# Kernel tuning notes

Measured on AMD Instinct MI355X. Metric: run time of the kernel, lower is better.

## Reference

```python
import jax, jax.numpy as jnp
import numpy as np

N_HEAD = 16
SCALE = float(np.sqrt(1024 // N_HEAD))  # source multiplies by sqrt(head_dim) (faithful to bug)


def setup_inputs() -> dict:
    key = jax.random.key(0)
    ks = jax.random.split(key, 4)
    B, T, D = 4, 2048, 1024
    std = 1.0 / np.sqrt(D)
    return {
        "x": jax.random.normal(ks[0], (B, T, D), dtype=jnp.float32),
        "Wq": jax.random.normal(ks[1], (D, D), dtype=jnp.float32) * std,
        "bq": jnp.zeros((D,), dtype=jnp.float32),
        "Wk": jax.random.normal(ks[2], (D, D), dtype=jnp.float32) * std,
        "bk": jnp.zeros((D,), dtype=jnp.float32),
        "Wv": jax.random.normal(ks[3], (D, D), dtype=jnp.float32) * std,
        "bv": jnp.zeros((D,), dtype=jnp.float32),
    }


def reference(x, Wq, bq, Wk, bk, Wv, bv):
    B, T, D = x.shape
    H = N_HEAD
    hd = D // H
    # linear projections (torch Linear: x @ W^T + b)
    q = x @ Wq.T + bq
    k = x @ Wk.T + bk
    v = x @ Wv.T + bv
    # [B, H, T, hd]
    q = q.reshape(B, T, H, hd).transpose(0, 2, 1, 3)
    k = k.reshape(B, T, H, hd).transpose(0, 2, 1, 3)
    v = v.reshape(B, T, H, hd).transpose(0, 2, 1, 3)
    # scores [B, H, T, T]; note: source MULTIPLIES by sqrt(head_dim)
    att = jnp.einsum("bhqd,bhkd->bhqk", q, k) * SCALE
    causal = jnp.tril(jnp.ones((T, T), dtype=bool))
    att = jnp.where(causal, att, -jnp.inf)
    att = jax.nn.softmax(att, axis=-1)
    y = jnp.einsum("bhqk,bhkd->bhqd", att, v)
    return y.transpose(0, 2, 1, 3).reshape(B, T, D)
```

## Files before the change

### kernel.cpp

```cpp
#include <hip/hip_runtime.h>
#include <math.h>

#define TSEQ   2048
#define NBATCH 4
#define NHEAD  16
#define HDIM   64
#define DMODEL 1024
#define MROWS  (NBATCH * TSEQ)
#define QSCALE 11.541560327111707f

typedef float f32x4  __attribute__((ext_vector_type(4)));
typedef short bf16x8 __attribute__((ext_vector_type(8)));
typedef _Float16 f16x8 __attribute__((ext_vector_type(8)));

static __device__ __forceinline__ short f2bf(float f) {
    union { float f; unsigned u; } a; a.f = f;
    unsigned r = a.u + 0x7FFFu + ((a.u >> 16) & 1u);
    return (short)(r >> 16);
}
static __device__ __forceinline__ float bf2f(short s) {
    union { unsigned u; float f; } a; a.u = ((unsigned)(unsigned short)s) << 16;
    return a.f;
}

static __device__ __forceinline__ void async_copy16(void* lds, const void* g) {
    __builtin_amdgcn_global_load_lds(
        (const __attribute__((address_space(1))) void*)g,
        (__attribute__((address_space(3))) void*)lds, 16, 0, 0);
}

#define X_F4 (MROWS * DMODEL / 4)
#define W_F4 (DMODEL * DMODEL / 4)
__global__ __launch_bounds__(256) void split_all(
    const float* __restrict__ x,
    const float* __restrict__ wq, const float* __restrict__ wk,
    const float* __restrict__ wv,
    short* __restrict__ Xhi, short* __restrict__ Xlo,
    short* __restrict__ Whi, short* __restrict__ Wlo)
{
    int gid = blockIdx.x * 256 + threadIdx.x;
    const float* src; short* dh; short* dl; int off;
    if (gid < X_F4) {
        src = x; dh = Xhi; dl = Xlo; off = gid;
    } else {
        int r = gid - X_F4;
        int z = r >> 18;
        off = r & (W_F4 - 1);
        src = (z == 0) ? wq : (z == 1) ? wk : wv;
        dh = Whi + (size_t)z * DMODEL * DMODEL;
        dl = Wlo + (size_t)z * DMODEL * DMODEL;
    }
    float4 v = ((const float4*)src)[off];
    float f[4] = {v.x, v.y, v.z, v.w};
    short h[4], l[4];
    #pragma unroll
    for (int c = 0; c < 4; c++) {
        h[c] = f2bf(f[c]);
        l[c] = f2bf(f[c] - bf2f(h[c]));
    }
    *(float2*)(dh + (size_t)off * 4) = *(const float2*)h;
    *(float2*)(dl + (size_t)off * 4) = *(const float2*)l;
}

__global__ __launch_bounds__(256, 2) void qkv_gemm_mfma(
    const short* __restrict__ Xhi, const short* __restrict__ Xlo,
    const short* __restrict__ Wh3, const short* __restrict__ Wl3,
    const float* __restrict__ bq, const float* __restrict__ bk,
    const float* __restrict__ bv,
    short* __restrict__ Qhi, short* __restrict__ Qlo,
    short* __restrict__ Khi, short* __restrict__ Klo,
    _Float16* __restrict__ VgT)
{
    const int z = blockIdx.z;
    const bool dolo = (z != 2);
    const short* Wh = Wh3 + (size_t)z * DMODEL * DMODEL;
    const short* Wl = Wl3 + (size_t)z * DMODEL * DMODEL;
    const float* bias = (z == 0) ? bq : (z == 1) ? bk : bv;

    __shared__ __align__(16) short Ah[128 * 32];
    __shared__ __align__(16) short Al[128 * 32];
    __shared__ __align__(16) short Bh[128 * 32];
    __shared__ __align__(16) short Bl[128 * 32];

    const int tid  = threadIdx.x;
    const int w    = tid >> 6;
    const int lane = tid & 63;
    const int t    = lane & 15;
    const int quad = lane >> 4;
    const int wm   = w >> 1, wn = w & 1;

    const int orig = blockIdx.x + (blockIdx.y << 3);
    const int nw   = (orig & 7) * 64 + (orig >> 3);
    const int bm   = (nw >> 3) * 128;
    const int bn   = (nw & 7) * 128;

    const int r_local = lane >> 2;
    const int kq      = (lane & 3) ^ ((r_local >> 1) & 3);
    const int row0    = w * 32 + r_local;
    const int slotq   = (quad ^ ((t >> 1) & 3)) * 8;

    f32x4 acc[4][4];
    #pragma unroll
    for (int i = 0; i < 4; i++)
        #pragma unroll
        for (int j = 0; j < 4; j++) acc[i][j] = (f32x4){0.f, 0.f, 0.f, 0.f};

    for (int k0 = 0; k0 < DMODEL; k0 += 32) {
        __syncthreads();
        #pragma unroll
        for (int i = 0; i < 2; i++) {
            int row = row0 + i * 16;
            size_t ga = (size_t)(bm + row) * DMODEL + k0 + kq * 8;
            size_t gb = (size_t)(bn + row) * DMODEL + k0 + kq * 8;
            int ldst = (w * 32 + i * 16) * 32;
            async_copy16(&Ah[ldst], Xhi + ga);
            async_copy16(&Bh[ldst], Wh + gb);
            if (dolo) {
                async_copy16(&Al[ldst], Xlo + ga);
                async_copy16(&Bl[ldst], Wl + gb);
            }
        }
        __syncthreads();

        bf16x8 ah[4], al[4], bh[4], bl[4];
        #pragma unroll
        for (int mt = 0; mt < 4; mt++) {
            int off = (wm * 64 + mt * 16 + t) * 32 + slotq;
            ah[mt] = *(const bf16x8*)&Ah[off];
            if (dolo) al[mt] = *(const bf16x8*)&Al[off];
        }
        #pragma unroll
        for (int nt = 0; nt < 4; nt++) {
            int off = (wn * 64 + nt * 16 + t) * 32 + slotq;
            bh[nt] = *(const bf16x8*)&Bh[off];
            if (dolo) bl[nt] = *(const bf16x8*)&Bl[off];
        }
        #pragma unroll
        for (int mt = 0; mt < 4; mt++)
            #pragma unroll
            for (int nt = 0; nt < 4; nt++) {
                if (dolo) {
                    acc[mt][nt] = __builtin_amdgcn_mfma_f32_16x16x32_bf16(
                        al[mt], bh[nt], acc[mt][nt], 0, 0, 0);
                    acc[mt][nt] = __builtin_amdgcn_mfma_f32_16x16x32_bf16(
                        ah[mt], bl[nt], acc[mt][nt], 0, 0, 0);
                }
                acc[mt][nt] = __builtin_amdgcn_mfma_f32_16x16x32_bf16(
                    ah[mt], bh[nt], acc[mt][nt], 0, 0, 0);
            }
    }

    const float scale = (z == 0) ? QSCALE : 1.0f;
    const int n_base = bn + wn * 64;
    const int h_head = n_base >> 6;
    float bvs[4];
    #pragma unroll
    for (int nt = 0; nt < 4; nt++)
        bvs[nt] = bias[n_base + nt * 16 + t];

    #pragma unroll
    for (int mt = 0; mt < 4; mt++) {
        #pragma unroll
        for (int r = 0; r < 4; r++) {
            int m  = bm + wm * 64 + mt * 16 + quad * 4 + r;
            int b_ = m >> 11;
            int t_ = m & 2047;
            #pragma unroll
            for (int nt = 0; nt < 4; nt++) {
                int d = nt * 16 + t;
                float v = (acc[mt][nt][r] + bvs[nt]) * scale;
                if (z == 2) {
                    size_t idx = ((size_t)(b_ * NHEAD + h_head) * HDIM + d) * TSEQ + t_;
                    VgT[idx] = (_Float16)v;
                } else {
                    size_t idx = (((size_t)(b_ * NHEAD + h_head) * TSEQ + t_) << 6) + d;
                    short hb = f2bf(v);
                    short lb = f2bf(v - bf2f(hb));
                    if (z == 0) { Qhi[idx] = hb; Qlo[idx] = lb; }
                    else        { Khi[idx] = hb; Klo[idx] = lb; }
                }
            }
        }
    }
}

__global__ __launch_bounds__(256, 2) void attn_fwd(
    const short* __restrict__ Qhi, const short* __restrict__ Qlo,
    const short* __restrict__ Khi, const short* __restrict__ Klo,
    const _Float16* __restrict__ VgT,
    float* __restrict__ out)
{
    __shared__ __align__(16) short    Kh_lds[2][64 * 64];
    __shared__ __align__(16) short    Kl_lds[2][64 * 64];
    __shared__ __align__(16) _Float16 Vt_lds[2][64 * 64];
    __shared__ __align__(16) _Float16 P_lds [128 * 72];

    const int tid  = threadIdx.x;

    const int orig = blockIdx.x + (blockIdx.y << 3);
    const int nw   = (orig & 7) * 64 + (orig >> 3);
    const int bh   = nw >> 3;
    const int xt   = nw & 7;

    const int b    = bh >> 4, h = bh & 15;
    const int w    = tid >> 6;
    const int lane = tid & 63;
    const int t    = lane & 15;
    const int quad = lane >> 4;

    const int rl      = w * 8 + (lane >> 3);
    const int chsw    = (lane & 7) ^ ((lane >> 3) & 7);
    const int ld_off  = (w * 8) * 64;

    const size_t kbase = (size_t)bh * TSEQ;
    const size_t vbase = (size_t)bh * HDIM;

    const int rs0 = ((0 * 4 + quad) ^ (t & 7)) * 8;
    const int rs1 = ((1 * 4 + quad) ^ (t & 7)) * 8;

    f16x8 ones;
    #pragma unroll
    for (int i = 0; i < 8; i++) ones[i] = (_Float16)1.0f;

    auto stage = [&](int kt, int bf) {
        #pragma unroll
        for (int i = 0; i < 2; i++) {
            int row = i * 32 + rl;
            const short* gk = Khi + (kbase + kt * 64 + row) * 64 + chsw * 8;
            async_copy16(&Kh_lds[bf][(i * 32) * 64 + ld_off], gk);
            const short* gl = Klo + (kbase + kt * 64 + row) * 64 + chsw * 8;
            async_copy16(&Kl_lds[bf][(i * 32) * 64 + ld_off], gl);
            const _Float16* gv = VgT + (vbase + row) * TSEQ + kt * 64 + chsw * 8;
            async_copy16(&Vt_lds[bf][(i * 32) * 64 + ld_off], gv);
        }
    };

    #pragma unroll 1
    for (int seg = 0; seg < 2; seg++) {
        const int qb = seg ? (15 - xt) : xt;

        bf16x8 qh[2][2], ql[2][2];
        #pragma unroll
        for (int mt = 0; mt < 2; mt++) {
            size_t qrow = kbase + qb * 128 + w * 32 + mt * 16 + t;
            #pragma unroll
            for (int dh = 0; dh < 2; dh++) {
                qh[mt][dh] = *(const bf16x8*)(Qhi + qrow * 64 + dh * 32 + quad * 8);
                ql[mt][dh] = *(const bf16x8*)(Qlo + qrow * 64 + dh * 32 + quad * 8);
            }
        }

        f32x4 O[2][4], Ol[2];
        #pragma unroll
        for (int mt = 0; mt < 2; mt++) {
            Ol[mt] = (f32x4){0.f, 0.f, 0.f, 0.f};
            #pragma unroll
            for (int j = 0; j < 4; j++) O[mt][j] = (f32x4){0.f, 0.f, 0.f, 0.f};
        }
        float m_st[2][4];
        #pragma unroll
        for (int mt = 0; mt < 2; mt++)
            #pragma unroll
            for (int r = 0; r < 4; r++) m_st[mt][r] = -1e30f;

        const int npair = qb + 1;

        #pragma unroll 1
        for (int p = 0; p < npair; p++) {
            __syncthreads();
            stage(2 * p, 0);
            stage(2 * p + 1, 1);
            __syncthreads();

            #pragma unroll
            for (int mt = 0; mt < 2; mt++) {
                f32x4 S[8];
                __builtin_amdgcn_s_setprio(1);
                #pragma unroll
                for (int c8 = 0; c8 < 8; c8++) {
                    S[c8] = (f32x4){0.f, 0.f, 0.f, 0.f};
                    const int bf = c8 >> 2;
                    const int rowoff = ((c8 & 3) * 16 + t) * 64;
                    {
                        bf16x8 kh = *(const bf16x8*)&Kh_lds[bf][rowoff + rs0];
                        bf16x8 kl = *(const bf16x8*)&Kl_lds[bf][rowoff + rs0];
                        S[c8] = __builtin_amdgcn_mfma_f32_16x16x32_bf16(ql[mt][0], kh, S[c8], 0, 0, 0);
                        S[c8] = __builtin_amdgcn_mfma_f32_16x16x32_bf16(qh[mt][0], kl, S[c8], 0, 0, 0);
                        S[c8] = __builtin_amdgcn_mfma_f32_16x16x32_bf16(qh[mt][0], kh, S[c8], 0, 0, 0);
                    }
                    {
                        bf16x8 kh = *(const bf16x8*)&Kh_lds[bf][rowoff + rs1];
                        bf16x8 kl = *(const bf16x8*)&Kl_lds[bf][rowoff + rs1];
                        S[c8] = __builtin_amdgcn_mfma_f32_16x16x32_bf16(ql[mt][1], kh, S[c8], 0, 0, 0);
                        S[c8] = __builtin_amdgcn_mfma_f32_16x16x32_bf16(qh[mt][1], kl, S[c8], 0, 0, 0);
                        S[c8] = __builtin_amdgcn_mfma_f32_16x16x32_bf16(qh[mt][1], kh, S[c8], 0, 0, 0);
                    }
                }
                __builtin_amdgcn_s_setprio(0);

                if (p == qb) {
                    #pragma unroll
                    for (int c8 = 0; c8 < 8; c8++) {
                        int col = c8 * 16 + t;
                        #pragma unroll
                        for (int r = 0; r < 4; r++)
                            if (col > w * 32 + mt * 16 + quad * 4 + r) S[c8][r] = -1e30f;
                    }
                }

                float mx[4]; bool grow = false;
                #pragma unroll
                for (int r = 0; r < 4; r++) {
                    float a0 = fmaxf(fmaxf(S[0][r], S[1][r]), fmaxf(S[2][r], S[3][r]));
                    float a1 = fmaxf(fmaxf(S[4][r], S[5][r]), fmaxf(S[6][r], S[7][r]));
                    float v = fmaxf(a0, a1);
                    v = fmaxf(v, __shfl_xor(v, 1, 64));
                    v = fmaxf(v, __shfl_xor(v, 2, 64));
                    v = fmaxf(v, __shfl_xor(v, 4, 64));
                    v = fmaxf(v, __shfl_xor(v, 8, 64));
                    mx[r] = v;
                    grow = grow || (v > m_st[mt][r]);
                }
                if (__ballot(grow)) {
                    #pragma unroll
                    for (int r = 0; r < 4; r++) {
                        float mn = fmaxf(m_st[mt][r], mx[r]);
                        float al = exp2f(m_st[mt][r] - mn);
                        m_st[mt][r] = mn;
                        Ol[mt][r] *= al;
                        #pragma unroll
                        for (int ct2 = 0; ct2 < 4; ct2++) O[mt][ct2][r] *= al;
                    }
                }
                #pragma unroll
                for (int c8 = 0; c8 < 8; c8++)
                    #pragma unroll
                    for (int r = 0; r < 4; r++)
                        S[c8][r] = exp2f(S[c8][r] - m_st[mt][r]);

                const int prow = w * 32 + mt * 16;
                #pragma unroll
                for (int half = 0; half < 2; half++) {
                    #pragma unroll
                    for (int ct = 0; ct < 4; ct++)
                        #pragma unroll
                        for (int r = 0; r < 4; r++)
                            P_lds[(prow + quad * 4 + r) * 72 + ct * 16 + t] =
                                (_Float16)S[half * 4 + ct][r];
                    f16x8 p0 = *(const f16x8*)&P_lds[(prow + t) * 72 + quad * 8];
                    f16x8 p1 = *(const f16x8*)&P_lds[(prow + t) * 72 + 32 + quad * 8];
                    __builtin_amdgcn_s_setprio(1);
                    #pragma unroll
                    for (int ct2 = 0; ct2 < 4; ct2++) {
                        int rowoff2 = (ct2 * 16 + t) * 64;
                        f16x8 v0 = *(const f16x8*)&Vt_lds[half][rowoff2 + rs0];
                        f16x8 v1 = *(const f16x8*)&Vt_lds[half][rowoff2 + rs1];
                        O[mt][ct2] = __builtin_amdgcn_mfma_f32_16x16x32_f16(p0, v0, O[mt][ct2], 0, 0, 0);
                        O[mt][ct2] = __builtin_amdgcn_mfma_f32_16x16x32_f16(p1, v1, O[mt][ct2], 0, 0, 0);
                    }
                    Ol[mt] = __builtin_amdgcn_mfma_f32_16x16x32_f16(p0, ones, Ol[mt], 0, 0, 0);
                    Ol[mt] = __builtin_amdgcn_mfma_f32_16x16x32_f16(p1, ones, Ol[mt], 0, 0, 0);
                    __builtin_amdgcn_s_setprio(0);
                }
            }
        }

        #pragma unroll
        for (int mt = 0; mt < 2; mt++) {
            float* ob = out + ((size_t)b * TSEQ + qb * 128 + w * 32 + mt * 16 + quad * 4) * DMODEL
                      + h * 64;
            #pragma unroll
            for (int r = 0; r < 4; r++) {
                float inv = 1.0f / Ol[mt][r];
                #pragma unroll
                for (int ct2 = 0; ct2 < 4; ct2++)
                    ob[(size_t)r * DMODEL + ct2 * 16 + t] = O[mt][ct2][r] * inv;
            }
        }
    }
}

extern "C" void kernel_launch(void* const* d_in, const int* in_sizes, int n_in,
                              void* d_out, int out_size, void* d_ws, size_t ws_size,
                              hipStream_t stream)
{
    const float* x  = (const float*)d_in[0];
    const float* Wq = (const float*)d_in[1];
    const float* bq = (const float*)d_in[2];
    const float* Wk = (const float*)d_in[3];
    const float* bk = (const float*)d_in[4];
    const float* Wv = (const float*)d_in[5];
    const float* bv = (const float*)d_in[6];

    const size_t TEN = (size_t)MROWS * DMODEL;
    const size_t WEN = (size_t)DMODEL * DMODEL;
    short* Xhi = (short*)d_ws;
    short* Xlo = Xhi + TEN;
    short* Whi = Xlo + TEN;
    short* Wlo = Whi + 3 * WEN;
    short* Qhi = Wlo + 3 * WEN;
    short* Qlo = Qhi + TEN;
    short* Khi = Qlo + TEN;
    short* Klo = Khi + TEN;
    _Float16* VgT = (_Float16*)(Klo + TEN);
    float* out = (float*)d_out;

    int nsplit = (X_F4 + 3 * W_F4) / 256;
    split_all<<<nsplit, 256, 0, stream>>>(x, Wq, Wk, Wv, Xhi, Xlo, Whi, Wlo);

    dim3 gg(DMODEL / 128, MROWS / 128, 3);
    qkv_gemm_mfma<<<gg, 256, 0, stream>>>(Xhi, Xlo, Whi, Wlo, bq, bk, bv,
                                          Qhi, Qlo, Khi, Klo, VgT);

    dim3 ga(8, NBATCH * NHEAD);
    attn_fwd<<<ga, 256, 0, stream>>>(Qhi, Qlo, Khi, Klo, VgT, out);
}
```

Measured before the change: 360.7 us.

## Compute transposed scores to keep P in registers, dropping LDS round-trip

Swaps the MFMA operand order so the S tile is produced transposed, with each lane holding one query row. That lets the row max reduce mostly in-register. P is then packed to fp16 and rearranged with cross-lane shuffles into the A-operand layout for the PV MFMA, instead of being written to and reread from a shared-memory buffer. It also adds a lazy rescale that updates the running max only when it grows by more than 8 (log2 units); this relies on fp16 headroom for P values above 1 and adds a small accuracy risk.

Result: faster. 349.8 us (-3.0%).

```diff
diff --git a/kernel.cpp b/kernel.cpp
--- a/kernel.cpp
+++ b/kernel.cpp
@@ -21,6 +21,11 @@
 static __device__ __forceinline__ float bf2f(short s) {
     union { unsigned u; float f; } a; a.u = ((unsigned)(unsigned short)s) << 16;
     return a.f;
+}
+static __device__ __forceinline__ unsigned pkh(float a, float b) {
+    union { _Float16 h[2]; unsigned u; } z;
+    z.h[0] = (_Float16)a; z.h[1] = (_Float16)b;
+    return z.u;
 }
 
 static __device__ __forceinline__ void async_copy16(void* lds, const void* g) {
@@ -193,7 +198,6 @@
     __shared__ __align__(16) short    Kh_lds[2][64 * 64];
     __shared__ __align__(16) short    Kl_lds[2][64 * 64];
     __shared__ __align__(16) _Float16 Vt_lds[2][64 * 64];
-    __shared__ __align__(16) _Float16 P_lds [128 * 72];
 
     const int tid  = threadIdx.x;
 
@@ -217,6 +221,10 @@
 
     const int rs0 = ((0 * 4 + quad) ^ (t & 7)) * 8;
     const int rs1 = ((1 * 4 + quad) ^ (t & 7)) * 8;
+    const int qsw = ((quad & 1) << 1) | (quad >> 1);
+    const int rp0 = ((0 * 4 + qsw) ^ (t & 7)) * 8;
+    const int rp1 = ((1 * 4 + qsw) ^ (t & 7)) * 8;
+    const bool hi4 = (quad & 1);
 
     f16x8 ones;
     #pragma unroll
@@ -257,11 +265,8 @@
             #pragma unroll
             for (int j = 0; j < 4; j++) O[mt][j] = (f32x4){0.f, 0.f, 0.f, 0.f};
         }
-        float m_st[2][4];
-        #pragma unroll
-        for (int mt = 0; mt < 2; mt++)
-            #pragma unroll
-            for (int r = 0; r < 4; r++) m_st[mt][r] = -1e30f;
+        float m_st[2];
+        m_st[0] = -1e30f; m_st[1] = -1e30f;
 
         const int npair = qb + 1;
 
@@ -284,82 +289,96 @@
                     {
                         bf16x8 kh = *(const bf16x8*)&Kh_lds[bf][rowoff + rs0];
                         bf16x8 kl = *(const bf16x8*)&Kl_lds[bf][rowoff + rs0];
-                        S[c8] = __builtin_amdgcn_mfma_f32_16x16x32_bf16(ql[mt][0], kh, S[c8], 0, 0, 0);
-                        S[c8] = __builtin_amdgcn_mfma_f32_16x16x32_bf16(qh[mt][0], kl, S[c8], 0, 0, 0);
-                        S[c8] = __builtin_amdgcn_mfma_f32_16x16x32_bf16(qh[mt][0], kh, S[c8], 0, 0, 0);
+                        S[c8] = __builtin_amdgcn_mfma_f32_16x16x32_bf16(kh, ql[mt][0], S[c8], 0, 0, 0);
+                        S[c8] = __builtin_amdgcn_mfma_f32_16x16x32_bf16(kl, qh[mt][0], S[c8], 0, 0, 0);
+                        S[c8] = __builtin_amdgcn_mfma_f32_16x16x32_bf16(kh, qh[mt][0], S[c8], 0, 0, 0);
                     }
                     {
                         bf16x8 kh = *(const bf16x8*)&Kh_lds[bf][rowoff + rs1];
                         bf16x8 kl = *(const bf16x8*)&Kl_lds[bf][rowoff + rs1];
-                        S[c8] = __builtin_amdgcn_mfma_f32_16x16x32_bf16(ql[mt][1], kh, S[c8], 0, 0, 0);
-                        S[c8] = __builtin_amdgcn_mfma_f32_16x16x32_bf16(qh[mt][1], kl, S[c8], 0, 0, 0);
-                        S[c8] = __builtin_amdgcn_mfma_f32_16x16x32_bf16(qh[mt][1], kh, S[c8], 0, 0, 0);
+                        S[c8] = __builtin_amdgcn_mfma_f32_16x16x32_bf16(kh, ql[mt][1], S[c8], 0, 0, 0);
+                        S[c8] = __builtin_amdgcn_mfma_f32_16x16x32_bf16(kl, qh[mt][1], S[c8], 0, 0, 0);
+                        S[c8] = __builtin_amdgcn_mfma_f32_16x16x32_bf16(kh, qh[mt][1], S[c8], 0, 0, 0);
                     }
                 }
                 __builtin_amdgcn_s_setprio(0);
 
                 if (p == qb) {
+                    const int qloc = w * 32 + mt * 16 + t;
                     #pragma unroll
                     for (int c8 = 0; c8 < 8; c8++) {
-                        int col = c8 * 16 + t;
+                        int kp = c8 * 16 + quad * 4;
                         #pragma unroll
                         for (int r = 0; r < 4; r++)
-                            if (col > w * 32 + mt * 16 + quad * 4 + r) S[c8][r] = -1e30f;
-                    }
-                }
-
-                float mx[4]; bool grow = false;
-                #pragma unroll
-                for (int r = 0; r < 4; r++) {
-                    float a0 = fmaxf(fmaxf(S[0][r], S[1][r]), fmaxf(S[2][r], S[3][r]));
-                    float a1 = fmaxf(fmaxf(S[4][r], S[5][r]), fmaxf(S[6][r], S[7][r]));
-                    float v = fmaxf(a0, a1);
-                    v = fmaxf(v, __shfl_xor(v, 1, 64));
-                    v = fmaxf(v, __shfl_xor(v, 2, 64));
-                    v = fmaxf(v, __shfl_xor(v, 4, 64));
-                    v = fmaxf(v, __shfl_xor(v, 8, 64));
-                    mx[r] = v;
-                    grow = grow || (v > m_st[mt][r]);
-                }
-                if (__ballot(grow)) {
+                            if (kp + r > qloc) S[c8][r] = -1e30f;
+                    }
+                }
+
+                float mx = S[0][0];
+                #pragma unroll
+                for (int c8 = 0; c8 < 8; c8++)
+                    #pragma unroll
+                    for (int r = 0; r < 4; r++)
+                        mx = fmaxf(mx, S[c8][r]);
+                mx = fmaxf(mx, __shfl_xor(mx, 16));
+                mx = fmaxf(mx, __shfl_xor(mx, 32));
+
+                bool need = mx > m_st[mt] + 8.0f;
+                if (__ballot(need)) {
+                    float mn = fmaxf(m_st[mt], mx);
+                    float al = exp2f(m_st[mt] - mn);
+                    m_st[mt] = mn;
                     #pragma unroll
                     for (int r = 0; r < 4; r++) {
-                        float mn = fmaxf(m_st[mt][r], mx[r]);
-                        float al = exp2f(m_st[mt][r] - mn);
-                        m_st[mt][r] = mn;
-                        Ol[mt][r] *= al;
+                        float a = __shfl(al, (lane & 48) + quad * 4 + r);
+                        Ol[mt][r] *= a;
                         #pragma unroll
-                        for (int ct2 = 0; ct2 < 4; ct2++) O[mt][ct2][r] *= al;
-                    }
-                }
+                        for (int ct2 = 0; ct2 < 4; ct2++) O[mt][ct2][r] *= a;
+                    }
+                }
+
                 #pragma unroll
                 for (int c8 = 0; c8 < 8; c8++)
                     #pragma unroll
                     for (int r = 0; r < 4; r++)
-                        S[c8][r] = exp2f(S[c8][r] - m_st[mt][r]);
-
-                const int prow = w * 32 + mt * 16;
-                #pragma unroll
-                for (int half = 0; half < 2; half++) {
-                    #pragma unroll
-                    for (int ct = 0; ct < 4; ct++)
-                        #pragma unroll
-                        for (int r = 0; r < 4; r++)
-                            P_lds[(prow + quad * 4 + r) * 72 + ct * 16 + t] =
-                                (_Float16)S[half * 4 + ct][r];
-                    f16x8 p0 = *(const f16x8*)&P_lds[(prow + t) * 72 + quad * 8];
-                    f16x8 p1 = *(const f16x8*)&P_lds[(prow + t) * 72 + 32 + quad * 8];
+                        S[c8][r] = exp2f(S[c8][r] - m_st[mt]);
+
+                unsigned P2[8][2];
+                #pragma unroll
+                for (int c8 = 0; c8 < 8; c8++) {
+                    P2[c8][0] = pkh(S[c8][0], S[c8][1]);
+                    P2[c8][1] = pkh(S[c8][2], S[c8][3]);
+                }
+
+                unsigned FR[4][4];
+                #pragma unroll
+                for (int tau = 0; tau < 4; tau++) {
+                    #pragma unroll
+                    for (int rp = 0; rp < 2; rp++) {
+                        unsigned X  = P2[2 * tau][rp];
+                        unsigned Y  = P2[2 * tau + 1][rp];
+                        unsigned Xs = (unsigned)__shfl_xor((int)X, 16);
+                        unsigned Ys = (unsigned)__shfl_xor((int)Y, 16);
+                        FR[tau][rp]     = hi4 ? Ys : X;
+                        FR[tau][2 + rp] = hi4 ? Y  : Xs;
+                    }
+                }
+
+                #pragma unroll
+                for (int tau = 0; tau < 4; tau++) {
+                    union { unsigned u[4]; f16x8 v; } pu;
+                    pu.u[0] = FR[tau][0]; pu.u[1] = FR[tau][1];
+                    pu.u[2] = FR[tau][2]; pu.u[3] = FR[tau][3];
+                    f16x8 pf = pu.v;
+                    const int bf  = tau >> 1;
+                    const int rsP = (tau & 1) ? rp1 : rp0;
                     __builtin_amdgcn_s_setprio(1);
                     #pragma unroll
                     for (int ct2 = 0; ct2 < 4; ct2++) {
-                        int rowoff2 = (ct2 * 16 + t) * 64;
-                        f16x8 v0 = *(const f16x8*)&Vt_lds[half][rowoff2 + rs0];
-                        f16x8 v1 = *(const f16x8*)&Vt_lds[half][rowoff2 + rs1];
-                        O[mt][ct2] = __builtin_amdgcn_mfma_f32_16x16x32_f16(p0, v0, O[mt][ct2], 0, 0, 0);
-                        O[mt][ct2] = __builtin_amdgcn_mfma_f32_16x16x32_f16(p1, v1, O[mt][ct2], 0, 0, 0);
-                    }
-                    Ol[mt] = __builtin_amdgcn_mfma_f32_16x16x32_f16(p0, ones, Ol[mt], 0, 0, 0);
-                    Ol[mt] = __builtin_amdgcn_mfma_f32_16x16x32_f16(p1, ones, Ol[mt], 0, 0, 0);
+                        f16x8 v = *(const f16x8*)&Vt_lds[bf][(ct2 * 16 + t) * 64 + rsP];
+                        O[mt][ct2] = __builtin_amdgcn_mfma_f32_16x16x32_f16(pf, v, O[mt][ct2], 0, 0, 0);
+                    }
+                    Ol[mt] = __builtin_amdgcn_mfma_f32_16x16x32_f16(pf, ones, Ol[mt], 0, 0, 0);
                     __builtin_amdgcn_s_setprio(0);
                 }
             }
```
